# Performance work log

Measured on AMD Instinct MI355X. Metric: run time of the kernel, lower is better.

Reference implementation:

```python
import jax, jax.numpy as jnp
import numpy as np

EMBED = 960
NUM_CLASSES = 10
LN_EPS = 1e-5


def _linear_params(key, fan_in, fan_out):
    kw, kb = jax.random.split(key)
    bound = 1.0 / np.sqrt(fan_in)
    W = jax.random.uniform(kw, (fan_out, fan_in), jnp.float32, -bound, bound)
    b = jax.random.uniform(kb, (fan_out,), jnp.float32, -bound, bound)
    return W, b


def setup_inputs() -> dict:
    key = jax.random.key(0)
    ks = jax.random.split(key, 10)
    B, S, D = 32, 1024, EMBED
    x = jax.random.normal(ks[0], (B, S, D), jnp.float32)
    mask = jax.random.randint(ks[1], (B, S), 0, 2, jnp.int32)
    Wq, bq = _linear_params(ks[2], D, D)
    Wk, bk = _linear_params(ks[3], D, D)
    Wv, bv = _linear_params(ks[4], D, D)
    ln_g = jnp.ones((D,), jnp.float32)
    ln_b = jnp.zeros((D,), jnp.float32)
    W1, b1 = _linear_params(ks[5], D, 512)
    W2, b2 = _linear_params(ks[6], 512, 256)
    W3, b3 = _linear_params(ks[7], 256, 128)
    W4, b4 = _linear_params(ks[8], 128, NUM_CLASSES)
    return dict(x=x, mask=mask, Wq=Wq, bq=bq, Wk=Wk, bk=bk, Wv=Wv, bv=bv,
                ln_g=ln_g, ln_b=ln_b, W1=W1, b1=b1, W2=W2, b2=b2,
                W3=W3, b3=b3, W4=W4, b4=b4)


def reference(x, mask, Wq, bq, Wk, bk, Wv, bv, ln_g, ln_b,
              W1, b1, W2, b2, W3, b3, W4, b4):
    D = x.shape[-1]
    # single-head self-attention (hand-rolled, full NxN scores)
    Q = jnp.einsum('bsd,ed->bse', x, Wq) + bq
    K = jnp.einsum('bsd,ed->bse', x, Wk) + bk
    V = jnp.einsum('bsd,ed->bse', x, Wv) + bv
    scores = jnp.einsum('bqd,bkd->bqk', Q, K) / np.sqrt(D)  # [B,S,S]
    scores = jnp.where(mask[:, None, :] == 0, -1e9, scores)
    attn = jax.nn.softmax(scores, axis=-1)
    context = jnp.einsum('bqk,bkd->bqd', attn, V)
    # residual + LayerNorm
    h = context + x
    mu = jnp.mean(h, axis=-1, keepdims=True)
    var = jnp.mean(jnp.square(h - mu), axis=-1, keepdims=True)
    ctx = (h - mu) * jax.lax.rsqrt(var + LN_EPS) * ln_g + ln_b
    # masked mean pool
    mf = mask[:, :, None].astype(jnp.float32)  # [B,S,1]
    pooled = (ctx * mf).sum(axis=1) / jnp.clip(mf.sum(axis=1), 1e-9)
    # MLP (dropout inactive in eval mode)
    h = jax.nn.relu(pooled @ W1.T + b1)
    h = jax.nn.relu(h @ W2.T + b2)
    h = jax.nn.relu(h @ W3.T + b3)
    return h @ W4.T + b4
```

## Files before the change

### kernel.cpp

```cpp
#include <hip/hip_runtime.h>


#define DEVINL __device__ __forceinline__

typedef __attribute__((ext_vector_type(8))) short bf16x8;
typedef __attribute__((ext_vector_type(4))) float f32x4;
typedef __attribute__((ext_vector_type(4))) unsigned short u16x4;

DEVINL unsigned short f2bf(float f) {
  unsigned int u = __float_as_uint(f);
  u += 0x7FFFu + ((u >> 16) & 1u);
  return (unsigned short)(u >> 16);
}

DEVINL float bf2f(unsigned short h) { return __uint_as_float(((unsigned int)h) << 16); }

DEVINL void gload_lds16(const void* g, void* l) {
  __builtin_amdgcn_global_load_lds((const __attribute__((address_space(1))) unsigned int*)g,
                                   (__attribute__((address_space(3))) unsigned int*)l,
                                   16, 0, 0);
}

#define MFMA16(a, b, c) __builtin_amdgcn_mfma_f32_16x16x32_bf16((a), (b), (c), 0, 0, 0)

__global__ __launch_bounds__(256) void scan_mask(
    const int* __restrict__ mask, int* __restrict__ idx, int* __restrict__ cnt) {
  __shared__ int ps[256];
  const int b = blockIdx.x, t = threadIdx.x;
  const int4 m = *(const int4*)(mask + b * 1024 + t * 4);
  const int s = (m.x != 0) + (m.y != 0) + (m.z != 0) + (m.w != 0);
  ps[t] = s;
  __syncthreads();
  for (int off = 1; off < 256; off <<= 1) {
    const int v = (t >= off) ? ps[t - off] : 0;
    __syncthreads();
    ps[t] += v;
    __syncthreads();
  }
  int pos = ps[t] - s;
  if (m.x) idx[b * 1024 + pos++] = t * 4 + 0;
  if (m.y) idx[b * 1024 + pos++] = t * 4 + 1;
  if (m.z) idx[b * 1024 + pos++] = t * 4 + 2;
  if (m.w) idx[b * 1024 + pos++] = t * 4 + 3;
  if (t == 255) cnt[b] = ps[255];
}

__global__ __launch_bounds__(256) void cast_wqkv(
    const float* __restrict__ Wq, const float* __restrict__ Wk, const float* __restrict__ Wv,
    const float* __restrict__ bq, const float* __restrict__ bk, const float* __restrict__ bv,
    unsigned short* __restrict__ Wqkv, float* __restrict__ biasQ, float scaleQ) {
  const int r = blockIdx.x, t = threadIdx.x;
  const int seg = (r >= 1920) ? 2 : (r >= 960 ? 1 : 0);
  const int sr = r - seg * 960;
  const float* W = (seg == 0) ? Wq : (seg == 1) ? Wk : Wv;
  const float sc = (seg == 0) ? scaleQ : 1.0f;
  if (t < 240) {
    f32x4 v = *(const f32x4*)(W + (size_t)sr * 960 + t * 4);
    u16x4 o;
    o[0] = f2bf(v[0] * sc); o[1] = f2bf(v[1] * sc);
    o[2] = f2bf(v[2] * sc); o[3] = f2bf(v[3] * sc);
    *(u16x4*)(Wqkv + (size_t)r * 1024 + t * 4) = o;
  } else {
    u16x4 z = {};
    *(u16x4*)(Wqkv + (size_t)r * 1024 + 960 + (t - 240) * 4) = z;
  }
  if (t == 0) {
    const float* bb = (seg == 0) ? bq : (seg == 1) ? bk : bv;
    biasQ[r] = bb[sr] * sc;
  }
}

__global__ __launch_bounds__(256) void compact_x(
    const float* __restrict__ x, const int* __restrict__ idx, const int* __restrict__ cnt,
    unsigned short* __restrict__ xc) {
  const int b = blockIdx.y;
  const int j = blockIdx.x * 4 + (threadIdx.x >> 6);
  const int l = threadIdx.x & 63;
  const int cb = cnt[b];
  const int cbc = (cb + 127) & ~127;
  if (j >= cbc) return;
  unsigned short* o = xc + ((size_t)b * 1024 + j) * 1024 + l * 16;
  bf16x8 o0 = {}, o1 = {};
  if (j < cb && l < 60) {
    const int s = idx[b * 1024 + j];
    const float* g = x + ((size_t)b * 1024 + s) * 960 + l * 16;
    f32x4 v0 = *(const f32x4*)(g);
    f32x4 v1 = *(const f32x4*)(g + 4);
    f32x4 v2 = *(const f32x4*)(g + 8);
    f32x4 v3 = *(const f32x4*)(g + 12);
    o0[0] = (short)f2bf(v0[0]); o0[1] = (short)f2bf(v0[1]);
    o0[2] = (short)f2bf(v0[2]); o0[3] = (short)f2bf(v0[3]);
    o0[4] = (short)f2bf(v1[0]); o0[5] = (short)f2bf(v1[1]);
    o0[6] = (short)f2bf(v1[2]); o0[7] = (short)f2bf(v1[3]);
    o1[0] = (short)f2bf(v2[0]); o1[1] = (short)f2bf(v2[1]);
    o1[2] = (short)f2bf(v2[2]); o1[3] = (short)f2bf(v2[3]);
    o1[4] = (short)f2bf(v3[0]); o1[5] = (short)f2bf(v3[1]);
    o1[6] = (short)f2bf(v3[2]); o1[7] = (short)f2bf(v3[3]);
  }
  *(bf16x8*)(o) = o0;
  *(bf16x8*)(o + 8) = o1;
}

template <int MODE>
__global__ __launch_bounds__(256, 4) void gemm128s(
    const unsigned short* __restrict__ Ap, const unsigned short* __restrict__ Bp,
    int lda, int ldb, const float* __restrict__ bias,
    unsigned short* __restrict__ outC, unsigned short* __restrict__ outQ,
    unsigned short* __restrict__ outK, unsigned short* __restrict__ outV,
    int mTiles, int nTiles, int nktFixed, int ncols, int ldo,
    size_t aStride, size_t bStride, size_t oStride, const int* __restrict__ cntArr) {
  __shared__ unsigned short As[128 * 32];
  __shared__ unsigned short Bs[128 * 32];
  const int t = threadIdx.x, l = t & 63, w = t >> 6;
  const int wr = w >> 1, wc = w & 1;
  const int lq = l & 15, lh = l >> 4;

  const int nwg = (int)gridDim.x;
  const int flat = (int)blockIdx.x;
  const int q8 = nwg >> 3, r8 = nwg & 7, xcd = flat & 7;
  const int wgid = (xcd < r8 ? xcd * (q8 + 1) : r8 * (q8 + 1) + (xcd - r8) * q8) + (flat >> 3);
  const int pt = mTiles * nTiles;
  const int zb = wgid / pt;
  const int rm = wgid - zb * pt;
  const int mi = rm / nTiles;
  const int m0 = mi * 128;
  const int n0 = (rm - mi * nTiles) * 128;

  const int cb = cntArr[zb];
  if (m0 >= cb) return;
  const int nkt = (MODE == 2) ? ((cb + 31) >> 5) : nktFixed;

  const unsigned short* A = Ap + (size_t)zb * aStride + (size_t)m0 * lda;
  const unsigned short* B = Bp + (size_t)zb * bStride + (size_t)n0 * ldb;

  const int srow0 = w * 16 + (l >> 2);
  const int sg0 = l & 3;

  f32x4 acc[4][4] = {};
  for (int kt = 0; kt < nkt; ++kt) {
    const int d0 = kt * 32;
    __syncthreads();
#pragma unroll
    for (int p = 0; p < 2; ++p) {
      const int row = p * 64 + srow0;
      const int sg = sg0 ^ ((row >> 1) & 3);
      gload_lds16(A + (size_t)row * lda + d0 + sg * 8,
                  (char*)As + (size_t)(p * 64 + w * 16) * 64);
      gload_lds16(B + (size_t)row * ldb + d0 + sg * 8,
                  (char*)Bs + (size_t)(p * 64 + w * 16) * 64);
    }
    __syncthreads();
    bf16x8 aF[4], bF[4];
#pragma unroll
    for (int i = 0; i < 4; ++i) {
      const int rowA = 64 * wr + 16 * i + lq;
      aF[i] = *(const bf16x8*)(As + (size_t)rowA * 32 +
                               (size_t)(lh ^ ((rowA >> 1) & 3)) * 8);
      const int rowB = 64 * wc + 16 * i + lq;
      bF[i] = *(const bf16x8*)(Bs + (size_t)rowB * 32 +
                               (size_t)(lh ^ ((rowB >> 1) & 3)) * 8);
    }
#pragma unroll
    for (int i = 0; i < 4; ++i)
#pragma unroll
      for (int j = 0; j < 4; ++j) acc[i][j] = MFMA16(aF[i], bF[j], acc[i][j]);
  }

  if (MODE == 2) {
#pragma unroll
    for (int j = 0; j < 4; ++j) {
      const int col = n0 + 64 * wc + 16 * j + lq;
      if (col >= ncols) continue;
#pragma unroll
      for (int i = 0; i < 4; ++i)
#pragma unroll
        for (int r = 0; r < 4; ++r) {
          const int row = m0 + 64 * wr + 16 * i + 4 * lh + r;
          outC[(size_t)zb * oStride + (size_t)row * ldo + col] = f2bf(acc[i][j][r]);
        }
    }
  } else {
#pragma unroll
    for (int j = 0; j < 4; ++j) {
      const int col = n0 + 64 * wc + 16 * j + lq;
      if (col >= ncols) continue;
      const int seg = (col >= 1920) ? 2 : (col >= 960 ? 1 : 0);
      const int dcol = col - seg * 960;
      const float bv = bias[col];
#pragma unroll
      for (int i = 0; i < 4; ++i)
#pragma unroll
        for (int r = 0; r < 4; ++r) {
          const int row = m0 + 64 * wr + 16 * i + 4 * lh + r;
          const unsigned short v = f2bf(acc[i][j][r] + bv);
          if (seg == 0) outQ[((size_t)zb * 1024 + row) * 960 + dcol] = v;
          else if (seg == 1) outK[((size_t)zb * 1024 + row) * 960 + dcol] = v;
          else outV[((size_t)zb << 20) + ((size_t)dcol << 10) + row] = v;
        }
    }
  }
}

__global__ __launch_bounds__(512, 2) void attn_softmax(
    const unsigned short* __restrict__ Qb, const unsigned short* __restrict__ Kb,
    const int* __restrict__ cnt, unsigned short* __restrict__ P) {
  __shared__ unsigned short Ks[2][1024 * 32];
  __shared__ unsigned short Qs[2][64 * 32];
  __shared__ float red[2][8][64];
  const int t = threadIdx.x, l = t & 63, w = t >> 6;
  const int flat = blockIdx.x;
  const int b = (flat & 7) * 4 + ((flat >> 3) >> 4);
  const int q0 = ((flat >> 3) & 15) * 64;
  const int cb = cnt[b];
  if (q0 >= cb) return;
  const int nks = (cb + 127) >> 7;
  const int lq = l & 15, lh = l >> 4;
  const size_t kbase = (size_t)b * 1024 * 960;
  const size_t qbase = ((size_t)b * 1024 + q0) * 960;
  const int lr = l >> 2, sg0 = l & 3;

#define STAGE(kkv, bufv)                                                      \
  {                                                                           \
    const int d0_ = (kkv) * 32;                                               \
    _Pragma("unroll") for (int i_ = 0; i_ < 8; ++i_) {                        \
      const int br_ = i_ * 128 + w * 16;                                      \
      const int kr_ = (i_ < nks) ? (br_ + lr) : (w * 16 + lr);                \
      const int sg_ = sg0 ^ ((kr_ >> 1) & 3);                                 \
      gload_lds16(Kb + kbase + (size_t)kr_ * 960 + d0_ + sg_ * 8,             \
                  (char*)Ks[(bufv)] + (size_t)br_ * 64);                      \
    }                                                                         \
    {                                                                         \
      const int qw_ = w & 3;                                                  \
      const int qr_ = qw_ * 16 + lr;                                          \
      const int sg_ = sg0 ^ ((qr_ >> 1) & 3);                                 \
      gload_lds16(Qb + qbase + (size_t)qr_ * 960 + d0_ + sg_ * 8,             \
                  (char*)Qs[(bufv)] + (size_t)(qw_ * 16) * 64);               \
    }                                                                         \
  }

  f32x4 acc[4][8] = {};
  STAGE(0, 0);
  int buf = 0;
  for (int kk = 0; kk < 30; ++kk) {
    if (kk < 29) {
      STAGE(kk + 1, buf ^ 1);
      asm volatile("s_waitcnt vmcnt(9)" ::: "memory");
    } else {
      asm volatile("s_waitcnt vmcnt(0)" ::: "memory");
    }
    __builtin_amdgcn_sched_barrier(0);
    __builtin_amdgcn_s_barrier();
    if (w < nks) {
      bf16x8 aF[4], bF[8];
#pragma unroll
      for (int i = 0; i < 4; ++i) {
        const int qr = 16 * i + lq;
        aF[i] = *(const bf16x8*)(Qs[buf] + qr * 32 + (lh ^ ((qr >> 1) & 3)) * 8);
      }
#pragma unroll
      for (int j = 0; j < 8; ++j) {
        const int kr = 128 * w + 16 * j + lq;
        bF[j] = *(const bf16x8*)(Ks[buf] + kr * 32 + (lh ^ ((kr >> 1) & 3)) * 8);
      }
#pragma unroll
      for (int i = 0; i < 4; ++i)
#pragma unroll
        for (int j = 0; j < 8; ++j) acc[i][j] = MFMA16(aF[i], bF[j], acc[i][j]);
    }
    __builtin_amdgcn_s_barrier();
    buf ^= 1;
  }
#undef STAGE

#pragma unroll
  for (int j = 0; j < 8; ++j) {
    const int k = 128 * w + 16 * j + lq;
    if (k >= cb) {
#pragma unroll
      for (int i = 0; i < 4; ++i)
#pragma unroll
        for (int r = 0; r < 4; ++r) acc[i][j][r] = -1e9f;
    }
  }

  float rmax[4][4];
#pragma unroll
  for (int i = 0; i < 4; ++i)
#pragma unroll
    for (int r = 0; r < 4; ++r) {
      float m = acc[i][0][r];
#pragma unroll
      for (int j = 1; j < 8; ++j) m = fmaxf(m, acc[i][j][r]);
      m = fmaxf(m, __shfl_xor(m, 1));
      m = fmaxf(m, __shfl_xor(m, 2));
      m = fmaxf(m, __shfl_xor(m, 4));
      m = fmaxf(m, __shfl_xor(m, 8));
      rmax[i][r] = m;
    }
  if (lq == 0) {
#pragma unroll
    for (int i = 0; i < 4; ++i)
#pragma unroll
      for (int r = 0; r < 4; ++r) red[0][w][16 * i + 4 * lh + r] = rmax[i][r];
  }
  __syncthreads();
#pragma unroll
  for (int i = 0; i < 4; ++i)
#pragma unroll
    for (int r = 0; r < 4; ++r) {
      const int rowi = 16 * i + 4 * lh + r;
      float m = red[0][0][rowi];
#pragma unroll
      for (int w2 = 1; w2 < 8; ++w2) m = fmaxf(m, red[0][w2][rowi]);
      rmax[i][r] = m;
    }

  float rsum[4][4];
#pragma unroll
  for (int i = 0; i < 4; ++i)
#pragma unroll
    for (int r = 0; r < 4; ++r) {
      float s = 0.f;
#pragma unroll
      for (int j = 0; j < 8; ++j) {
        const float e = __expf(acc[i][j][r] - rmax[i][r]);
        acc[i][j][r] = e;
        s += e;
      }
      s += __shfl_xor(s, 1); s += __shfl_xor(s, 2);
      s += __shfl_xor(s, 4); s += __shfl_xor(s, 8);
      rsum[i][r] = s;
    }
  if (lq == 0) {
#pragma unroll
    for (int i = 0; i < 4; ++i)
#pragma unroll
      for (int r = 0; r < 4; ++r) red[1][w][16 * i + 4 * lh + r] = rsum[i][r];
  }
  __syncthreads();

  if (w < nks) {
    const size_t pb = ((size_t)b << 20) + (size_t)q0 * 1024;
#pragma unroll
    for (int i = 0; i < 4; ++i)
#pragma unroll
      for (int r = 0; r < 4; ++r) {
        const int rowi = 16 * i + 4 * lh + r;
        float s = 0.f;
#pragma unroll
        for (int w2 = 0; w2 < 8; ++w2) s += red[1][w2][rowi];
        const float inv = 1.0f / s;
#pragma unroll
        for (int j = 0; j < 8; ++j) {
          const int col = 128 * w + 16 * j + lq;
          P[pb + (size_t)rowi * 1024 + col] = f2bf(acc[i][j][r] * inv);
        }
      }
  }
}

__global__ __launch_bounds__(256) void ln_pool(
    const unsigned short* __restrict__ ctxb, const float* __restrict__ x,
    const int* __restrict__ idx, const int* __restrict__ cnt,
    const float* __restrict__ g, const float* __restrict__ bta,
    float* __restrict__ pooled) {
  const int b = blockIdx.y, chunk = blockIdx.x;
  const int w = threadIdx.x >> 6, l = threadIdx.x & 63;
  const int cb = cnt[b];
  f32x4 gc[4], bc[4];
#pragma unroll
  for (int c = 0; c < 4; ++c) {
    const int i4 = c * 64 + l;
    if (i4 < 240) {
      gc[c] = *(const f32x4*)(g + i4 * 4);
      bc[c] = *(const f32x4*)(bta + i4 * 4);
    }
  }
  f32x4 accp[4] = {};
  for (int rr = 0; rr < 8; ++rr) {
    const int j = chunk * 32 + w * 8 + rr;
    if (j >= cb) continue;
    const int sidx = idx[b * 1024 + j];
    const size_t cbase = ((size_t)b * 1024 + j) * 960;
    const size_t xbase = ((size_t)b * 1024 + sidx) * 960;
    f32x4 h[4];
    float part = 0.f;
#pragma unroll
    for (int c = 0; c < 4; ++c) {
      const int i4 = c * 64 + l;
      if (i4 < 240) {
        u16x4 cv = *(const u16x4*)(ctxb + cbase + (size_t)i4 * 4);
        f32x4 xv = *(const f32x4*)(x + xbase + (size_t)i4 * 4);
        h[c][0] = bf2f(cv[0]) + xv[0];
        h[c][1] = bf2f(cv[1]) + xv[1];
        h[c][2] = bf2f(cv[2]) + xv[2];
        h[c][3] = bf2f(cv[3]) + xv[3];
        part += h[c][0] + h[c][1] + h[c][2] + h[c][3];
      } else {
        h[c] = 0;
      }
    }
#pragma unroll
    for (int o = 1; o < 64; o <<= 1) part += __shfl_xor(part, o);
    const float mu = part * (1.0f / 960.0f);
    float p2 = 0.f;
#pragma unroll
    for (int c = 0; c < 4; ++c) {
      if (c * 64 + l < 240) {
#pragma unroll
        for (int k2 = 0; k2 < 4; ++k2) {
          const float d = h[c][k2] - mu;
          p2 += d * d;
        }
      }
    }
#pragma unroll
    for (int o = 1; o < 64; o <<= 1) p2 += __shfl_xor(p2, o);
    const float rs = rsqrtf(p2 * (1.0f / 960.0f) + 1e-5f);
#pragma unroll
    for (int c = 0; c < 4; ++c) {
      if (c * 64 + l < 240) {
#pragma unroll
        for (int k2 = 0; k2 < 4; ++k2)
          accp[c][k2] += (h[c][k2] - mu) * rs * gc[c][k2] + bc[c][k2];
      }
    }
  }
#pragma unroll
  for (int c = 0; c < 4; ++c) {
    const int i4 = c * 64 + l;
    if (i4 < 240) {
#pragma unroll
      for (int k2 = 0; k2 < 4; ++k2) atomicAdd(&pooled[b * 960 + i4 * 4 + k2], accp[c][k2]);
    }
  }
}

__global__ __launch_bounds__(256) void mlp_head(
    const float* __restrict__ pooled, const int* __restrict__ cnt,
    const float* __restrict__ W1, const float* __restrict__ b1,
    const float* __restrict__ W2, const float* __restrict__ b2,
    const float* __restrict__ W3, const float* __restrict__ b3,
    const float* __restrict__ W4, const float* __restrict__ b4, float* __restrict__ out) {
  __shared__ float h0[960], h1[512], h2[256], h3[128];
  const int b = blockIdx.x, t = threadIdx.x;
  const float inv = 1.0f / fmaxf((float)cnt[b], 1e-9f);
  for (int d = t; d < 960; d += 256) h0[d] = pooled[b * 960 + d] * inv;
  __syncthreads();
  for (int o = t; o < 512; o += 256) {
    float a = b1[o];
    const float* wr = W1 + (size_t)o * 960;
    for (int k = 0; k < 960; k += 4) {
      f32x4 wv = *(const f32x4*)(wr + k);
      f32x4 hv = *(const f32x4*)(h0 + k);
      a += wv[0] * hv[0] + wv[1] * hv[1] + wv[2] * hv[2] + wv[3] * hv[3];
    }
    h1[o] = fmaxf(a, 0.f);
  }
  __syncthreads();
  {
    float a = b2[t];
    const float* wr = W2 + (size_t)t * 512;
    for (int k = 0; k < 512; k += 4) {
      f32x4 wv = *(const f32x4*)(wr + k);
      f32x4 hv = *(const f32x4*)(h1 + k);
      a += wv[0] * hv[0] + wv[1] * hv[1] + wv[2] * hv[2] + wv[3] * hv[3];
    }
    h2[t] = fmaxf(a, 0.f);
  }
  __syncthreads();
  if (t < 128) {
    float a = b3[t];
    const float* wr = W3 + (size_t)t * 256;
    for (int k = 0; k < 256; k += 4) {
      f32x4 wv = *(const f32x4*)(wr + k);
      f32x4 hv = *(const f32x4*)(h2 + k);
      a += wv[0] * hv[0] + wv[1] * hv[1] + wv[2] * hv[2] + wv[3] * hv[3];
    }
    h3[t] = fmaxf(a, 0.f);
  }
  __syncthreads();
  if (t < 10) {
    float a = b4[t];
    const float* wr = W4 + (size_t)t * 128;
    for (int k = 0; k < 128; ++k) a += wr[k] * h3[k];
    out[b * 10 + t] = a;
  }
}

extern "C" void kernel_launch(void* const* d_in, const int* in_sizes, int n_in,
                              void* d_out, int out_size, void* d_ws, size_t ws_size,
                              hipStream_t stream) {
  (void)in_sizes; (void)n_in; (void)out_size; (void)ws_size;
  const float* x    = (const float*)d_in[0];
  const int*   mask = (const int*)d_in[1];
  const float* Wq   = (const float*)d_in[2];
  const float* bq   = (const float*)d_in[3];
  const float* Wk   = (const float*)d_in[4];
  const float* bk   = (const float*)d_in[5];
  const float* Wv   = (const float*)d_in[6];
  const float* bv   = (const float*)d_in[7];
  const float* lng  = (const float*)d_in[8];
  const float* lnb  = (const float*)d_in[9];
  const float* W1   = (const float*)d_in[10];
  const float* b1   = (const float*)d_in[11];
  const float* W2   = (const float*)d_in[12];
  const float* b2   = (const float*)d_in[13];
  const float* W3   = (const float*)d_in[14];
  const float* b3   = (const float*)d_in[15];
  const float* W4   = (const float*)d_in[16];
  const float* b4   = (const float*)d_in[17];
  float* out = (float*)d_out;

  char* ws = (char*)d_ws;
  unsigned short* xc     = (unsigned short*)(ws);
  unsigned short* P      = (unsigned short*)(ws);
  unsigned short* Qb     = (unsigned short*)(ws + 67108864);
  unsigned short* Kb     = (unsigned short*)(ws + 130023424);
  unsigned short* ctxb   = (unsigned short*)(ws + 67108864);
  unsigned short* Vt     = (unsigned short*)(ws + 192937984);
  unsigned short* Wqkv   = (unsigned short*)(ws + 260046848);
  float*          biasQ  = (float*)(ws + 266338304);
  float*          pooled = (float*)(ws + 266349824);
  int*            cntW   = (int*)(ws + 266472704);
  int*            idxW   = (int*)(ws + 266472832);

  const float scaleQ = 0.0322748612183951f;

  scan_mask<<<32, 256, 0, stream>>>(mask, idxW, cntW);
  cast_wqkv<<<2880, 256, 0, stream>>>(Wq, Wk, Wv, bq, bk, bv, Wqkv, biasQ, scaleQ);
  compact_x<<<dim3(256, 32), 256, 0, stream>>>(x, idxW, cntW, xc);

  gemm128s<1><<<32 * 8 * 23, 256, 0, stream>>>(
      xc, Wqkv, 1024, 1024, biasQ, nullptr, Qb, Kb, Vt,
      8, 23, 30, 2880, 0, (size_t)1048576, 0, 0, cntW);

  attn_softmax<<<512, 512, 0, stream>>>(Qb, Kb, cntW, P);

  gemm128s<2><<<8 * 8 * 32, 256, 0, stream>>>(
      P, Vt, 1024, 1024, nullptr, ctxb, nullptr, nullptr, nullptr,
      8, 8, 0, 960, 960, (size_t)1048576, (size_t)1048576, (size_t)983040, cntW);

  hipMemsetAsync(pooled, 0, 32 * 960 * 4, stream);
  ln_pool<<<dim3(32, 32), 256, 0, stream>>>(ctxb, x, idxW, cntW, lng, lnb, pooled);
  mlp_head<<<32, 256, 0, stream>>>(pooled, cntW, W1, b1, W2, b2, W3, b3, W4, b4, out);
}
```

Baseline: 503.1 us.

## Specialize attention K-loop on active key-slab count and vectorize V stores

The QK^T loop is templated on the number of active 128-key slabs, so blocks with few valid keys load only the K rows they need instead of always issuing eight loads per stage with redundant re-fetches. The vmcnt wait is adjusted per specialization to match the reduced load count. The V transpose store in the QKV projection epilogue now writes four contiguous bf16 values at once instead of scalar stores. This adds code size through five template instantiations and relies on the mask-derived key count falling in 3..6 for the fast paths.

New measurement: 459.0 us, median of 2. -8.8%, faster.

```diff
diff --git a/kernel.cpp b/kernel.cpp
--- a/kernel.cpp
+++ b/kernel.cpp
@@ -187,18 +187,94 @@
       const int seg = (col >= 1920) ? 2 : (col >= 960 ? 1 : 0);
       const int dcol = col - seg * 960;
       const float bv = bias[col];
+      if (seg == 2) {
+#pragma unroll
+        for (int i = 0; i < 4; ++i) {
+          const int row = m0 + 64 * wr + 16 * i + 4 * lh;
+          u16x4 v4;
+          v4[0] = f2bf(acc[i][j][0] + bv);
+          v4[1] = f2bf(acc[i][j][1] + bv);
+          v4[2] = f2bf(acc[i][j][2] + bv);
+          v4[3] = f2bf(acc[i][j][3] + bv);
+          *(u16x4*)(outV + ((size_t)zb << 20) + ((size_t)dcol << 10) + row) = v4;
+        }
+      } else {
+#pragma unroll
+        for (int i = 0; i < 4; ++i)
+#pragma unroll
+          for (int r = 0; r < 4; ++r) {
+            const int row = m0 + 64 * wr + 16 * i + 4 * lh + r;
+            const unsigned short v = f2bf(acc[i][j][r] + bv);
+            if (seg == 0) outQ[((size_t)zb * 1024 + row) * 960 + dcol] = v;
+            else outK[((size_t)zb * 1024 + row) * 960 + dcol] = v;
+          }
+      }
+    }
+  }
+}
+
+template <int NKS>
+DEVINL void attn_kloop(const unsigned short* __restrict__ Kp,
+                       const unsigned short* __restrict__ Qp,
+                       unsigned short (*Ks)[1024 * 32], unsigned short (*Qs)[64 * 32],
+                       int w, int lr, int sg0, int lq, int lh, int nks_rt,
+                       f32x4 (&acc)[4][8]) {
+#define STG(kkv, bufv)                                                        \
+  {                                                                           \
+    const int d0_ = (kkv) * 32;                                               \
+    _Pragma("unroll") for (int i_ = 0; i_ < NKS; ++i_) {                      \
+      const int br_ = i_ * 128 + w * 16;                                      \
+      const int kr_ = (NKS == 8) ? ((i_ < nks_rt) ? (br_ + lr) : (w * 16 + lr)) \
+                                 : (br_ + lr);                                \
+      const int sg_ = sg0 ^ ((kr_ >> 1) & 3);                                 \
+      gload_lds16(Kp + (size_t)kr_ * 960 + d0_ + sg_ * 8,                     \
+                  (char*)Ks[(bufv)] + (size_t)br_ * 64);                      \
+    }                                                                         \
+    {                                                                         \
+      const int qw_ = w & 3;                                                  \
+      const int qr_ = qw_ * 16 + lr;                                          \
+      const int sg_ = sg0 ^ ((qr_ >> 1) & 3);                                 \
+      gload_lds16(Qp + (size_t)qr_ * 960 + d0_ + sg_ * 8,                     \
+                  (char*)Qs[(bufv)] + (size_t)(qw_ * 16) * 64);               \
+    }                                                                         \
+  }
+  STG(0, 0);
+  int buf = 0;
+  const int gate = (NKS == 8) ? nks_rt : NKS;
+  for (int kk = 0; kk < 30; ++kk) {
+    if (kk < 29) {
+      STG(kk + 1, buf ^ 1);
+      if constexpr (NKS == 3)      asm volatile("s_waitcnt vmcnt(4)" ::: "memory");
+      else if constexpr (NKS == 4) asm volatile("s_waitcnt vmcnt(5)" ::: "memory");
+      else if constexpr (NKS == 5) asm volatile("s_waitcnt vmcnt(6)" ::: "memory");
+      else if constexpr (NKS == 6) asm volatile("s_waitcnt vmcnt(7)" ::: "memory");
+      else                         asm volatile("s_waitcnt vmcnt(9)" ::: "memory");
+    } else {
+      asm volatile("s_waitcnt vmcnt(0)" ::: "memory");
+    }
+    __builtin_amdgcn_sched_barrier(0);
+    __builtin_amdgcn_s_barrier();
+    if (w < gate) {
+      bf16x8 aF[4], bF[8];
+#pragma unroll
+      for (int i = 0; i < 4; ++i) {
+        const int qr = 16 * i + lq;
+        aF[i] = *(const bf16x8*)(Qs[buf] + qr * 32 + (lh ^ ((qr >> 1) & 3)) * 8);
+      }
+#pragma unroll
+      for (int j = 0; j < 8; ++j) {
+        const int kr = 128 * w + 16 * j + lq;
+        bF[j] = *(const bf16x8*)(Ks[buf] + kr * 32 + (lh ^ ((kr >> 1) & 3)) * 8);
+      }
 #pragma unroll
       for (int i = 0; i < 4; ++i)
 #pragma unroll
-        for (int r = 0; r < 4; ++r) {
-          const int row = m0 + 64 * wr + 16 * i + 4 * lh + r;
-          const unsigned short v = f2bf(acc[i][j][r] + bv);
-          if (seg == 0) outQ[((size_t)zb * 1024 + row) * 960 + dcol] = v;
-          else if (seg == 1) outK[((size_t)zb * 1024 + row) * 960 + dcol] = v;
-          else outV[((size_t)zb << 20) + ((size_t)dcol << 10) + row] = v;
-        }
-    }
-  }
+        for (int j = 0; j < 8; ++j) acc[i][j] = MFMA16(aF[i], bF[j], acc[i][j]);
+    }
+    __builtin_amdgcn_s_barrier();
+    buf ^= 1;
+  }
+#undef STG
 }
 
 __global__ __launch_bounds__(512, 2) void attn_softmax(
@@ -215,62 +291,16 @@
   if (q0 >= cb) return;
   const int nks = (cb + 127) >> 7;
   const int lq = l & 15, lh = l >> 4;
-  const size_t kbase = (size_t)b * 1024 * 960;
-  const size_t qbase = ((size_t)b * 1024 + q0) * 960;
+  const unsigned short* Kp = Kb + (size_t)b * 1024 * 960;
+  const unsigned short* Qp = Qb + ((size_t)b * 1024 + q0) * 960;
   const int lr = l >> 2, sg0 = l & 3;
 
-#define STAGE(kkv, bufv)                                                      \
-  {                                                                           \
-    const int d0_ = (kkv) * 32;                                               \
-    _Pragma("unroll") for (int i_ = 0; i_ < 8; ++i_) {                        \
-      const int br_ = i_ * 128 + w * 16;                                      \
-      const int kr_ = (i_ < nks) ? (br_ + lr) : (w * 16 + lr);                \
-      const int sg_ = sg0 ^ ((kr_ >> 1) & 3);                                 \
-      gload_lds16(Kb + kbase + (size_t)kr_ * 960 + d0_ + sg_ * 8,             \
-                  (char*)Ks[(bufv)] + (size_t)br_ * 64);                      \
-    }                                                                         \
-    {                                                                         \
-      const int qw_ = w & 3;                                                  \
-      const int qr_ = qw_ * 16 + lr;                                          \
-      const int sg_ = sg0 ^ ((qr_ >> 1) & 3);                                 \
-      gload_lds16(Qb + qbase + (size_t)qr_ * 960 + d0_ + sg_ * 8,             \
-                  (char*)Qs[(bufv)] + (size_t)(qw_ * 16) * 64);               \
-    }                                                                         \
-  }
-
   f32x4 acc[4][8] = {};
-  STAGE(0, 0);
-  int buf = 0;
-  for (int kk = 0; kk < 30; ++kk) {
-    if (kk < 29) {
-      STAGE(kk + 1, buf ^ 1);
-      asm volatile("s_waitcnt vmcnt(9)" ::: "memory");
-    } else {
-      asm volatile("s_waitcnt vmcnt(0)" ::: "memory");
-    }
-    __builtin_amdgcn_sched_barrier(0);
-    __builtin_amdgcn_s_barrier();
-    if (w < nks) {
-      bf16x8 aF[4], bF[8];
-#pragma unroll
-      for (int i = 0; i < 4; ++i) {
-        const int qr = 16 * i + lq;
-        aF[i] = *(const bf16x8*)(Qs[buf] + qr * 32 + (lh ^ ((qr >> 1) & 3)) * 8);
-      }
-#pragma unroll
-      for (int j = 0; j < 8; ++j) {
-        const int kr = 128 * w + 16 * j + lq;
-        bF[j] = *(const bf16x8*)(Ks[buf] + kr * 32 + (lh ^ ((kr >> 1) & 3)) * 8);
-      }
-#pragma unroll
-      for (int i = 0; i < 4; ++i)
-#pragma unroll
-        for (int j = 0; j < 8; ++j) acc[i][j] = MFMA16(aF[i], bF[j], acc[i][j]);
-    }
-    __builtin_amdgcn_s_barrier();
-    buf ^= 1;
-  }
-#undef STAGE
+  if (nks == 4)      attn_kloop<4>(Kp, Qp, Ks, Qs, w, lr, sg0, lq, lh, nks, acc);
+  else if (nks == 5) attn_kloop<5>(Kp, Qp, Ks, Qs, w, lr, sg0, lq, lh, nks, acc);
+  else if (nks == 3) attn_kloop<3>(Kp, Qp, Ks, Qs, w, lr, sg0, lq, lh, nks, acc);
+  else if (nks == 6) attn_kloop<6>(Kp, Qp, Ks, Qs, w, lr, sg0, lq, lh, nks, acc);
+  else               attn_kloop<8>(Kp, Qp, Ks, Qs, w, lr, sg0, lq, lh, nks, acc);
 
 #pragma unroll
   for (int j = 0; j < 8; ++j) {
```
